# Kernel optimization log

Measured on AMD Instinct MI355X. Metric: run time of the kernel, lower is better.

The kernel has to match this reference:

```python
import jax, jax.numpy as jnp
import numpy as np
import math

DIM = 384
HEADS = 6
HEAD_DIM = DIM // HEADS
MLP_HIDDEN = int(DIM * 2.0)


def layer_norm(x, g, b, eps=1e-5):
    mu = jnp.mean(x, axis=-1, keepdims=True)
    var = jnp.mean((x - mu) ** 2, axis=-1, keepdims=True)
    return (x - mu) * jax.lax.rsqrt(var + eps) * g + b


def setup_inputs() -> dict:
    key = jax.random.key(0)
    ks = jax.random.split(key, 12)
    B, N = 4, 2048
    s = 0.02
    return {
        "x": jax.random.normal(ks[0], (B, N, DIM), dtype=jnp.float32),
        "pos": jax.random.normal(ks[1], (B, N, 3), dtype=jnp.float32),
        "qkv_w": jax.random.normal(ks[2], (DIM, 3 * DIM), dtype=jnp.float32) * s,
        "qkv_b": jnp.zeros((3 * DIM,), jnp.float32),
        "proj_w": jax.random.normal(ks[3], (DIM, DIM), dtype=jnp.float32) * s,
        "proj_b": jnp.zeros((DIM,), jnp.float32),
        "mlp_w1": jax.random.normal(ks[4], (DIM, MLP_HIDDEN), dtype=jnp.float32) * s,
        "mlp_b1": jnp.zeros((MLP_HIDDEN,), jnp.float32),
        "mlp_w2": jax.random.normal(ks[5], (MLP_HIDDEN, DIM), dtype=jnp.float32) * s,
        "mlp_b2": jnp.zeros((DIM,), jnp.float32),
        "ln1_g": jnp.ones((DIM,), jnp.float32),
        "ln1_b": jnp.zeros((DIM,), jnp.float32),
        "ln2_g": jnp.ones((DIM,), jnp.float32),
        "ln2_b": jnp.zeros((DIM,), jnp.float32),
    }


def reference(x, pos, qkv_w, qkv_b, proj_w, proj_b, mlp_w1, mlp_b1,
              mlp_w2, mlp_b2, ln1_g, ln1_b, ln2_g, ln2_b):
    B, N, D = x.shape
    H, Hd = HEADS, HEAD_DIM
    # qkv projection
    qkv = layer_norm(x, ln1_g, ln1_b) @ qkv_w + qkv_b          # [B,N,3D]
    qkv = qkv.reshape(B, N, 3, H, Hd)
    q = jnp.transpose(qkv[:, :, 0], (0, 2, 1, 3))               # [B,H,N,Hd]
    k = jnp.transpose(qkv[:, :, 1], (0, 2, 1, 3))
    v = jnp.transpose(qkv[:, :, 2], (0, 2, 1, 3))
    # pairwise squared-distance bias: exp(-||p_i - p_j||^2)
    rel = pos[:, :, None, :] - pos[:, None, :, :]               # [B,N,N,3]
    dist = jnp.exp(-jnp.sum(rel ** 2, axis=-1))                 # [B,N,N]
    scale = 1.0 / math.sqrt(Hd)
    attn = jnp.einsum('bhqd,bhkd->bhqk', q, k) * scale + dist[:, None, :, :]
    attn = jax.nn.softmax(attn, axis=-1)
    out = jnp.einsum('bhqk,bhkd->bhqd', attn, v)                # [B,H,N,Hd]
    out = jnp.transpose(out, (0, 2, 1, 3)).reshape(B, N, D)
    out = out @ proj_w + proj_b
    x = x + out
    h = layer_norm(x, ln2_g, ln2_b)
    h = jax.nn.gelu(h @ mlp_w1 + mlp_b1, approximate=False) @ mlp_w2 + mlp_b2
    return x + h
```

## Files before the change

kernel.cpp:

```cpp
#include <hip/hip_runtime.h>
#include <hip/hip_bf16.h>
#include <math.h>

#define DIMD 384
#define NHEADS 6
#define HD 64
#define MLPH 768
#define SEQ 2048
#define NBATCH 4
#define NTOK (NBATCH*SEQ)

typedef __hip_bfloat16 bf16;

typedef __attribute__((ext_vector_type(8))) short bf16x8;
typedef __attribute__((ext_vector_type(4))) float f32x4;

#define LOG2E 1.44269504088896340736f

static __device__ inline float fexp2(float x) { return __builtin_amdgcn_exp2f(x); }

static __device__ inline f32x4 mfma16(bf16x8 a, bf16x8 b, f32x4 c) {
    return __builtin_amdgcn_mfma_f32_16x16x32_bf16(a, b, c, 0, 0, 0);
}

static __device__ inline unsigned int cvtpk(float lo, float hi) {
    unsigned int r;
    asm("v_cvt_pk_bf16_f32 %0, %1, %2" : "=v"(r) : "v"(lo), "v"(hi));
    return r;
}
static __device__ inline float bflo(unsigned int u) { return __builtin_bit_cast(float, u << 16); }
static __device__ inline float bfhi(unsigned int u) { return __builtin_bit_cast(float, u & 0xffff0000u); }

static __device__ inline void gld16(const void* g, void* l) {
    __builtin_amdgcn_global_load_lds(
        (const __attribute__((address_space(1))) unsigned int*)g,
        (__attribute__((address_space(3))) unsigned int*)l, 16, 0, 0);
}

__global__ __launch_bounds__(256) void ln_k(const float* __restrict__ x,
                                            const float* __restrict__ gm,
                                            const float* __restrict__ bt,
                                            bf16* __restrict__ out) {
    int row = blockIdx.x * 4 + (threadIdx.x >> 6);
    int l = threadIdx.x & 63;
    const float* xr = x + (size_t)row * DIMD;
    float v[6];
#pragma unroll
    for (int j = 0; j < 6; ++j) v[j] = xr[l + 64 * j];
    float s = 0.f, s2 = 0.f;
#pragma unroll
    for (int j = 0; j < 6; ++j) { s += v[j]; s2 += v[j] * v[j]; }
#pragma unroll
    for (int m = 1; m < 64; m <<= 1) { s += __shfl_xor(s, m); s2 += __shfl_xor(s2, m); }
    float mu = s * (1.f / DIMD);
    float var = s2 * (1.f / DIMD) - mu * mu;
    float rs = rsqrtf(var + 1e-5f);
    bf16* orow = out + (size_t)row * DIMD;
#pragma unroll
    for (int j = 0; j < 6; ++j) {
        int i = l + 64 * j;
        orow[i] = __float2bfloat16((v[j] - mu) * rs * gm[i] + bt[i]);
    }
}

__global__ __launch_bounds__(256) void prep_k(const float* __restrict__ w1,
                                              const float* __restrict__ w2,
                                              const float* __restrict__ w3,
                                              const float* __restrict__ w4,
                                              bf16* __restrict__ o1,
                                              bf16* __restrict__ o2,
                                              bf16* __restrict__ o3,
                                              bf16* __restrict__ o4,
                                              const float* __restrict__ pos,
                                              bf16* __restrict__ DP,
                                              const float* __restrict__ x,
                                              const float* __restrict__ g1,
                                              const float* __restrict__ b1,
                                              bf16* __restrict__ xn) {
    __shared__ float t[32][33];
    int id = blockIdx.x;
    if (id < 1152) {
        const float* W; bf16* O; int K, N;
        if (id < 432)      { W = w1; O = o1; K = 384; N = 1152; }
        else if (id < 576) { W = w2; O = o2; K = 384; N = 384;  id -= 432; }
        else if (id < 864) { W = w3; O = o3; K = 384; N = 768;  id -= 576; }
        else               { W = w4; O = o4; K = 768; N = 384;  id -= 864; }
        int nbx = N >> 5;
        int nb = (id % nbx) * 32, kb = (id / nbx) * 32;
        int tx = threadIdx.x & 31, ty = threadIdx.x >> 5;
#pragma unroll
        for (int i = 0; i < 4; ++i)
            t[ty + 8 * i][tx] = W[(size_t)(kb + ty + 8 * i) * N + nb + tx];
        __syncthreads();
#pragma unroll
        for (int i = 0; i < 4; ++i)
            O[(size_t)(nb + ty + 8 * i) * K + kb + tx] = __float2bfloat16(t[tx][ty + 8 * i]);
    } else if (id < 1664) {
        int blk = id - 1152;
        int w = blk & 3, qt = (blk >> 2) & 31, b = blk >> 7;
        int l = threadIdx.x & 63, tt = threadIdx.x >> 6;
        int lq = l & 15, g = l >> 4;
        int q = qt * 64 + w * 16 + lq;
        const float* pq = pos + ((size_t)b * SEQ + q) * 3;
        float px = pq[0], py = pq[1], pz = pq[2];
        const float* posb = pos + (size_t)b * SEQ * 3;
        char* base = (char*)DP + (size_t)blk * 65536;
        for (int j = 0; j < 8; ++j) {
            int tt8 = tt * 8 + j;
#pragma unroll
            for (int m = 0; m < 2; ++m) {
                int k0 = tt8 * 64 + 32 * m + 4 * g;
                float a[24];
                const float* pk = posb + 3 * k0;
                *(f32x4*)&a[0]  = *(const f32x4*)pk;
                *(f32x4*)&a[4]  = *(const f32x4*)(pk + 4);
                *(f32x4*)&a[8]  = *(const f32x4*)(pk + 8);
                const float* pk2 = posb + 3 * (k0 + 16);
                *(f32x4*)&a[12] = *(const f32x4*)pk2;
                *(f32x4*)&a[16] = *(const f32x4*)(pk2 + 4);
                *(f32x4*)&a[20] = *(const f32x4*)(pk2 + 8);
                float o8[8];
#pragma unroll
                for (int r = 0; r < 8; ++r) {
                    float dx = px - a[3 * r], dy = py - a[3 * r + 1], dz = pz - a[3 * r + 2];
                    o8[r] = fexp2(-LOG2E * (dx * dx + dy * dy + dz * dz)) * LOG2E;
                }
                uint4 o;
                o.x = cvtpk(o8[0], o8[1]); o.y = cvtpk(o8[2], o8[3]);
                o.z = cvtpk(o8[4], o8[5]); o.w = cvtpk(o8[6], o8[7]);
                *(uint4*)(base + ((size_t)tt8 * 2 + m) * 1024 + l * 16) = o;
            }
        }
    } else {
        int row = (id - 1664) * 4 + (threadIdx.x >> 6);
        int l = threadIdx.x & 63;
        const float* xr = x + (size_t)row * DIMD;
        float v[6];
#pragma unroll
        for (int j = 0; j < 6; ++j) v[j] = xr[l + 64 * j];
        float s = 0.f, s2 = 0.f;
#pragma unroll
        for (int j = 0; j < 6; ++j) { s += v[j]; s2 += v[j] * v[j]; }
#pragma unroll
        for (int m = 1; m < 64; m <<= 1) { s += __shfl_xor(s, m); s2 += __shfl_xor(s2, m); }
        float mu = s * (1.f / DIMD);
        float var = s2 * (1.f / DIMD) - mu * mu;
        float rs = rsqrtf(var + 1e-5f);
        bf16* orow = xn + (size_t)row * DIMD;
#pragma unroll
        for (int j = 0; j < 6; ++j) {
            int i = l + 64 * j;
            orow[i] = __float2bfloat16((v[j] - mu) * rs * g1[i] + b1[i]);
        }
    }
}

template <int EPI>
__global__ __launch_bounds__(256) void gemm128_k(const bf16* __restrict__ A,
                                                 const bf16* __restrict__ WT,
                                                 const float* __restrict__ bias,
                                                 bf16* __restrict__ ob0,
                                                 bf16* __restrict__ ob1,
                                                 bf16* __restrict__ ob2,
                                                 int K, int Nw) {
    __shared__ __align__(16) char Als[2][8192];
    __shared__ __align__(16) char Bls[2][8192];
    int tid = threadIdx.x;
    int w = tid >> 6, l = tid & 63;
    int c = l & 15, g = l >> 4;
    int wr = w >> 1, wc = w & 1;
    int m0 = blockIdx.y * 128, n0 = blockIdx.x * 128;
    const char* Ag = (const char*)A + (size_t)m0 * K * 2;
    const char* Bg = (const char*)WT + (size_t)n0 * K * 2;
    int K2 = K * 2;

    f32x4 acc[4][4];
#pragma unroll
    for (int mi = 0; mi < 4; ++mi)
#pragma unroll
        for (int ni = 0; ni < 4; ++ni) acc[mi][ni] = (f32x4){0.f, 0.f, 0.f, 0.f};

    auto stage = [&](int t, int bi) {
#pragma unroll
        for (int p = 0; p < 2; ++p) {
            int chunk = p * 256 + tid;
            int r = chunk >> 2;
            int cc = ((chunk & 3) ^ (r & 3)) << 4;
            gld16(Ag + (size_t)r * K2 + t * 64 + cc, &Als[bi][chunk * 16]);
            gld16(Bg + (size_t)r * K2 + t * 64 + cc, &Bls[bi][chunk * 16]);
        }
    };

    stage(0, 0);
    int kcn = K >> 5;
    for (int t = 0; t < kcn; ++t) {
        int bi = t & 1;
        __syncthreads();
        if (t + 1 < kcn) stage(t + 1, bi ^ 1);
        bf16x8 af[4], bfr[4];
#pragma unroll
        for (int mi = 0; mi < 4; ++mi) {
            int row = wr * 64 + mi * 16 + c;
            __builtin_memcpy(&af[mi], &Als[bi][row * 64 + ((g ^ (row & 3)) << 4)], 16);
        }
#pragma unroll
        for (int ni = 0; ni < 4; ++ni) {
            int row = wc * 64 + ni * 16 + c;
            __builtin_memcpy(&bfr[ni], &Bls[bi][row * 64 + ((g ^ (row & 3)) << 4)], 16);
        }
#pragma unroll
        for (int mi = 0; mi < 4; ++mi)
#pragma unroll
            for (int ni = 0; ni < 4; ++ni)
                acc[mi][ni] = mfma16(af[mi], bfr[ni], acc[mi][ni]);
    }

#pragma unroll
    for (int mi = 0; mi < 4; ++mi) {
#pragma unroll
        for (int ni = 0; ni < 4; ++ni) {
            int ntb = n0 + wc * 64 + ni * 16;
#pragma unroll
            for (int r = 0; r < 4; ++r) {
                int m = m0 + wr * 64 + mi * 16 + 4 * g + r;
                int n = ntb + c;
                float val = acc[mi][ni][r] + bias[n];
                if (EPI == 0) {
                    int which = ntb / DIMD;
                    int rem = ntb - which * DIMD;
                    int h = rem >> 6;
                    int d = (rem & 63) + c;
                    int b = m >> 11, s = m & (SEQ - 1);
                    if (which == 2) {
                        int slot = (s & ~31) + 8 * ((m & 15) >> 2) + 4 * ((m >> 4) & 1) + (m & 3);
                        ob2[(((size_t)b * NHEADS + h) * HD + d) * SEQ + slot] = __float2bfloat16(val);
                    } else {
                        bf16* dp = which == 0 ? ob0 : ob1;
                        dp[(((size_t)b * NHEADS + h) * SEQ + s) * HD + d] = __float2bfloat16(val);
                    }
                } else {
                    float ge = 0.5f * val * (1.0f + erff(val * 0.70710678118654752f));
                    ob0[(size_t)m * Nw + n] = __float2bfloat16(ge);
                }
            }
        }
    }
}

template <int EPI>
__global__ __launch_bounds__(256) void gemm_k(const bf16* __restrict__ A,
                                              const bf16* __restrict__ WT,
                                              const float* __restrict__ bias,
                                              const float* __restrict__ resid,
                                              float* __restrict__ outf,
                                              int K, int Nw) {
    __shared__ __align__(16) char Als[2][8192];
    __shared__ __align__(16) char Bls[2][8192];
    int tid = threadIdx.x;
    int w = tid >> 6, l = tid & 63;
    int c = l & 15, g = l >> 4;
    int m0 = blockIdx.y * 64, n0 = blockIdx.x * 64;
    const char* Ag = (const char*)A + (size_t)m0 * K * 2;
    const char* Bg = (const char*)WT + (size_t)n0 * K * 2;
    int K2 = K * 2;

    f32x4 acc[4];
#pragma unroll
    for (int nt = 0; nt < 4; ++nt) acc[nt] = (f32x4){0.f, 0.f, 0.f, 0.f};

    auto stage = [&](int t, int bi) {
#pragma unroll
        for (int p = 0; p < 2; ++p) {
            int chunk = p * 256 + tid;
            int r = chunk >> 3;
            int cc = ((chunk & 7) ^ (r & 7)) << 4;
            gld16(Ag + (size_t)r * K2 + t * 128 + cc, &Als[bi][chunk * 16]);
            gld16(Bg + (size_t)r * K2 + t * 128 + cc, &Bls[bi][chunk * 16]);
        }
    };

    stage(0, 0);
    int kcn = K >> 6;
    int arow = (16 * w + c) * 128;
    int sw = c & 7;
    for (int t = 0; t < kcn; ++t) {
        int bi = t & 1;
        __syncthreads();
        if (t + 1 < kcn) stage(t + 1, bi ^ 1);
#pragma unroll
        for (int kk = 0; kk < 2; ++kk) {
            int ch = ((kk * 4 + g) ^ sw) << 4;
            bf16x8 af;
            __builtin_memcpy(&af, &Als[bi][arow + ch], 16);
#pragma unroll
            for (int nt = 0; nt < 4; ++nt) {
                bf16x8 bfr;
                __builtin_memcpy(&bfr, &Bls[bi][(nt * 16 + c) * 128 + ch], 16);
                acc[nt] = mfma16(af, bfr, acc[nt]);
            }
        }
    }

#pragma unroll
    for (int nt = 0; nt < 4; ++nt) {
        int ntb = n0 + nt * 16;
#pragma unroll
        for (int r = 0; r < 4; ++r) {
            int m = m0 + 16 * w + 4 * g + r;
            int n = ntb + c;
            float val = acc[nt][r] + bias[n];
            val += resid[(size_t)m * Nw + n];
            outf[(size_t)m * Nw + n] = val;
        }
    }
}

__global__ __launch_bounds__(256) void attn_k(const bf16* __restrict__ q,
                                              const bf16* __restrict__ k,
                                              const bf16* __restrict__ vT,
                                              const bf16* __restrict__ DP,
                                              bf16* __restrict__ out) {
    __shared__ __align__(16) char Kls[3][8192];
    __shared__ __align__(16) char Vls[3][8192];

    int tid = threadIdx.x;
    int w = tid >> 6, l = tid & 63;
    int lq = l & 15, g = l >> 4;
    int qt = blockIdx.x & 31;
    int bh = blockIdx.x >> 5;
    int b = bh / NHEADS, h = bh % NHEADS;
    int qrow = qt * 64 + w * 16 + lq;

    const bf16* qp = q + ((size_t)bh * SEQ + qrow) * HD + 8 * g;
    bf16x8 qf0 = *(const bf16x8*)qp;
    bf16x8 qf1 = *(const bf16x8*)(qp + 32);

    const char* kgb = (const char*)(k + (size_t)bh * SEQ * HD);
    const char* vgb = (const char*)(vT + (size_t)bh * HD * SEQ);
    const char* dpb = (const char*)DP + ((size_t)((b * 32 + qt) * 4 + w)) * 65536 + l * 16;

    const float SC2 = 0.125f * LOG2E;
    f32x4 oacc[4];
#pragma unroll
    for (int dt = 0; dt < 4; ++dt) oacc[dt] = (f32x4){0.f, 0.f, 0.f, 0.f};
    f32x4 osum = (f32x4){0.f, 0.f, 0.f, 0.f};
    bf16x8 ones = {(short)0x3F80, (short)0x3F80, (short)0x3F80, (short)0x3F80,
                   (short)0x3F80, (short)0x3F80, (short)0x3F80, (short)0x3F80};

    auto stage = [&](int t, int bi) {
#pragma unroll
        for (int p = 0; p < 2; ++p) {
            int chunk = p * 256 + tid;
            int r = chunk >> 3, c = chunk & 7;
            int cc = (c ^ (r & 7)) << 4;
            gld16(kgb + (size_t)t * 8192 + r * 128 + cc, &Kls[bi][chunk * 16]);
            gld16(vgb + (size_t)r * 4096 + t * 128 + cc, &Vls[bi][chunk * 16]);
        }
    };

    stage(0, 0);
    uint4 cdp0 = *(const uint4*)(dpb);
    uint4 cdp1 = *(const uint4*)(dpb + 1024);
    stage(1, 1);

    int ib0 = 0, ib1 = 1, ib2 = 2;
    int swq = lq & 7;
    for (int t = 0; t < 32; ++t) {
        asm volatile("s_waitcnt vmcnt(4)" ::: "memory");
        __builtin_amdgcn_sched_barrier(0);
        __builtin_amdgcn_s_barrier();
        __builtin_amdgcn_sched_barrier(0);

        f32x4 st[4];
        __builtin_amdgcn_s_setprio(1);
#pragma unroll
        for (int s = 0; s < 4; ++s) {
            int ro = (16 * s + lq) * 128;
            bf16x8 klo, khi;
            __builtin_memcpy(&klo, &Kls[ib0][ro + ((g ^ swq) << 4)], 16);
            __builtin_memcpy(&khi, &Kls[ib0][ro + (((4 + g) ^ swq) << 4)], 16);
            f32x4 z = (f32x4){0.f, 0.f, 0.f, 0.f};
            st[s] = mfma16(klo, qf0, z);
            st[s] = mfma16(khi, qf1, st[s]);
        }
        __builtin_amdgcn_s_setprio(0);

#pragma unroll
        for (int m = 0; m < 2; ++m) {
            uint4 cd = m == 0 ? cdp0 : cdp1;
            f32x4 s0v = st[2 * m], s1v = st[2 * m + 1];
            float p[8];
            p[0] = fexp2(s0v[0] * SC2 + bflo(cd.x));
            p[1] = fexp2(s0v[1] * SC2 + bfhi(cd.x));
            p[2] = fexp2(s0v[2] * SC2 + bflo(cd.y));
            p[3] = fexp2(s0v[3] * SC2 + bfhi(cd.y));
            p[4] = fexp2(s1v[0] * SC2 + bflo(cd.z));
            p[5] = fexp2(s1v[1] * SC2 + bfhi(cd.z));
            p[6] = fexp2(s1v[2] * SC2 + bflo(cd.w));
            p[7] = fexp2(s1v[3] * SC2 + bfhi(cd.w));

            unsigned int pw[4];
            pw[0] = cvtpk(p[0], p[1]);
            pw[1] = cvtpk(p[2], p[3]);
            pw[2] = cvtpk(p[4], p[5]);
            pw[3] = cvtpk(p[6], p[7]);
            bf16x8 pf;
            __builtin_memcpy(&pf, pw, 16);

            __builtin_amdgcn_s_setprio(1);
            osum = mfma16(ones, pf, osum);
#pragma unroll
            for (int dt = 0; dt < 4; ++dt) {
                int rv = (16 * dt + lq) * 128;
                bf16x8 vf;
                __builtin_memcpy(&vf, &Vls[ib0][rv + (((4 * m + g) ^ swq) << 4)], 16);
                oacc[dt] = mfma16(vf, pf, oacc[dt]);
            }
            __builtin_amdgcn_s_setprio(0);
        }

        __builtin_amdgcn_sched_barrier(0);
        int tn1 = t + 1 < 32 ? t + 1 : 31;
        const char* dpn = dpb + (size_t)tn1 * 2048;
        uint4 ndp0 = *(const uint4*)(dpn);
        uint4 ndp1 = *(const uint4*)(dpn + 1024);
        __builtin_amdgcn_sched_barrier(0);
        int tn2 = t + 2 < 32 ? t + 2 : 31;
        stage(tn2, ib2);
        __builtin_amdgcn_sched_barrier(0);
        cdp0 = ndp0; cdp1 = ndp1;
        int tmp = ib0; ib0 = ib1; ib1 = ib2; ib2 = tmp;
    }

    float inv = 1.f / osum[0];
    bf16* op = out + ((size_t)b * SEQ + qrow) * DIMD + h * HD + 4 * g;
#pragma unroll
    for (int dt = 0; dt < 4; ++dt) {
        unsigned int t2[2];
        t2[0] = cvtpk(oacc[dt][0] * inv, oacc[dt][1] * inv);
        t2[1] = cvtpk(oacc[dt][2] * inv, oacc[dt][3] * inv);
        __builtin_memcpy(op + dt * 16, t2, 8);
    }
}

extern "C" void kernel_launch(void* const* d_in, const int* in_sizes, int n_in,
                              void* d_out, int out_size, void* d_ws, size_t ws_size,
                              hipStream_t stream) {
    const float* x      = (const float*)d_in[0];
    const float* pos    = (const float*)d_in[1];
    const float* qkv_w  = (const float*)d_in[2];
    const float* qkv_b  = (const float*)d_in[3];
    const float* proj_w = (const float*)d_in[4];
    const float* proj_b = (const float*)d_in[5];
    const float* mlp_w1 = (const float*)d_in[6];
    const float* mlp_b1 = (const float*)d_in[7];
    const float* mlp_w2 = (const float*)d_in[8];
    const float* mlp_b2 = (const float*)d_in[9];
    const float* ln1_g  = (const float*)d_in[10];
    const float* ln1_b  = (const float*)d_in[11];
    const float* ln2_g  = (const float*)d_in[12];
    const float* ln2_b  = (const float*)d_in[13];

    char* p = (char*)d_ws;
    size_t off = 0;
    auto alloc = [&](size_t bytes) {
        char* r = p + off;
        off = (off + bytes + 255) & ~(size_t)255;
        return r;
    };
    bf16* WT1 = (bf16*)alloc((size_t)1152 * 384 * 2);
    bf16* WT2 = (bf16*)alloc((size_t)384 * 384 * 2);
    bf16* WT3 = (bf16*)alloc((size_t)384 * 768 * 2);
    bf16* WT4 = (bf16*)alloc((size_t)768 * 384 * 2);
    bf16* xn  = (bf16*)alloc((size_t)NTOK * DIMD * 2);
    bf16* xn2 = (bf16*)alloc((size_t)NTOK * DIMD * 2);
    bf16* qb  = (bf16*)alloc((size_t)NTOK * DIMD * 2);
    bf16* kb  = (bf16*)alloc((size_t)NTOK * DIMD * 2);
    bf16* vTb = (bf16*)alloc((size_t)NTOK * DIMD * 2);
    bf16* ao  = (bf16*)alloc((size_t)NTOK * DIMD * 2);
    float* x1 = (float*)alloc((size_t)NTOK * DIMD * 4);
    bf16* hh  = (bf16*)alloc((size_t)NTOK * MLPH * 2);
    bf16* dtab = (bf16*)alloc((size_t)NBATCH * SEQ * SEQ * 2);
    if (off > ws_size) return;

    prep_k<<<1152 + 512 + 2048, 256, 0, stream>>>(
        qkv_w, proj_w, mlp_w1, mlp_w2, WT1, WT2, WT3, WT4,
        pos, dtab, x, ln1_g, ln1_b, xn);

    gemm128_k<0><<<dim3(1152 / 128, NTOK / 128), 256, 0, stream>>>(
        xn, WT1, qkv_b, qb, kb, vTb, 384, 1152);
    attn_k<<<NBATCH * NHEADS * (SEQ / 64), 256, 0, stream>>>(qb, kb, vTb, dtab, ao);
    gemm_k<1><<<dim3(384 / 64, NTOK / 64), 256, 0, stream>>>(
        ao, WT2, proj_b, x, x1, 384, 384);
    ln_k<<<NTOK / 4, 256, 0, stream>>>(x1, ln2_g, ln2_b, xn2);
    gemm128_k<2><<<dim3(768 / 128, NTOK / 128), 256, 0, stream>>>(
        xn2, WT3, mlp_b1, hh, nullptr, nullptr, 384, 768);
    gemm_k<3><<<dim3(384 / 64, NTOK / 64), 256, 0, stream>>>(
        hh, WT4, mlp_b2, x1, (float*)d_out, 768, 384);
}
```

Baseline: 141.8 us.

## Register-tile two query tiles per wave in attention to reuse K/V LDS fragments

The attention kernel drops from 4 waves per block to 2, and each wave now handles 32 query rows (two 16-row tiles) instead of 16. Each K and V fragment read from LDS now feeds two MFMA streams, which halves LDS read traffic per MFMA. Staging loops and the vmcnt wait count are adjusted for the doubled per-thread copy work, and the unused EPI template parameter is removed from gemm_k. The trade-off is roughly double the accumulator and score registers per wave and half as many resident waves in total, which reduces latency hiding.

```diff
diff --git a/kernel.cpp b/kernel.cpp
--- a/kernel.cpp
+++ b/kernel.cpp
@@ -247,7 +247,6 @@
     }
 }
 
-template <int EPI>
 __global__ __launch_bounds__(256) void gemm_k(const bf16* __restrict__ A,
                                               const bf16* __restrict__ WT,
                                               const float* __restrict__ bias,
@@ -315,7 +314,7 @@
     }
 }
 
-__global__ __launch_bounds__(256) void attn_k(const bf16* __restrict__ q,
+__global__ __launch_bounds__(128) void attn_k(const bf16* __restrict__ q,
                                               const bf16* __restrict__ k,
                                               const bf16* __restrict__ vT,
                                               const bf16* __restrict__ DP,
@@ -329,49 +328,66 @@
     int qt = blockIdx.x & 31;
     int bh = blockIdx.x >> 5;
     int b = bh / NHEADS, h = bh % NHEADS;
-    int qrow = qt * 64 + w * 16 + lq;
-
-    const bf16* qp = q + ((size_t)bh * SEQ + qrow) * HD + 8 * g;
-    bf16x8 qf0 = *(const bf16x8*)qp;
-    bf16x8 qf1 = *(const bf16x8*)(qp + 32);
+    int qrowA = qt * 64 + w * 32 + lq;
+    int qrowB = qrowA + 16;
+
+    const bf16* qpA = q + ((size_t)bh * SEQ + qrowA) * HD + 8 * g;
+    bf16x8 qa0 = *(const bf16x8*)qpA;
+    bf16x8 qa1 = *(const bf16x8*)(qpA + 32);
+    const bf16* qpB = q + ((size_t)bh * SEQ + qrowB) * HD + 8 * g;
+    bf16x8 qb0 = *(const bf16x8*)qpB;
+    bf16x8 qb1 = *(const bf16x8*)(qpB + 32);
 
     const char* kgb = (const char*)(k + (size_t)bh * SEQ * HD);
     const char* vgb = (const char*)(vT + (size_t)bh * HD * SEQ);
-    const char* dpb = (const char*)DP + ((size_t)((b * 32 + qt) * 4 + w)) * 65536 + l * 16;
+    const char* dpA = (const char*)DP + ((size_t)((b * 32 + qt) * 4 + 2 * w)) * 65536 + l * 16;
+    const char* dpB = dpA + 65536;
 
     const float SC2 = 0.125f * LOG2E;
-    f32x4 oacc[4];
-#pragma unroll
-    for (int dt = 0; dt < 4; ++dt) oacc[dt] = (f32x4){0.f, 0.f, 0.f, 0.f};
-    f32x4 osum = (f32x4){0.f, 0.f, 0.f, 0.f};
+    f32x4 oaccA[4], oaccB[4];
+#pragma unroll
+    for (int dt = 0; dt < 4; ++dt) {
+        oaccA[dt] = (f32x4){0.f, 0.f, 0.f, 0.f};
+        oaccB[dt] = (f32x4){0.f, 0.f, 0.f, 0.f};
+    }
+    f32x4 osumA = (f32x4){0.f, 0.f, 0.f, 0.f};
+    f32x4 osumB = osumA;
     bf16x8 ones = {(short)0x3F80, (short)0x3F80, (short)0x3F80, (short)0x3F80,
                    (short)0x3F80, (short)0x3F80, (short)0x3F80, (short)0x3F80};
 
     auto stage = [&](int t, int bi) {
 #pragma unroll
-        for (int p = 0; p < 2; ++p) {
-            int chunk = p * 256 + tid;
+        for (int p = 0; p < 4; ++p) {
+            int chunk = p * 128 + tid;
             int r = chunk >> 3, c = chunk & 7;
             int cc = (c ^ (r & 7)) << 4;
             gld16(kgb + (size_t)t * 8192 + r * 128 + cc, &Kls[bi][chunk * 16]);
+        }
+#pragma unroll
+        for (int p = 0; p < 4; ++p) {
+            int chunk = p * 128 + tid;
+            int r = chunk >> 3, c = chunk & 7;
+            int cc = (c ^ (r & 7)) << 4;
             gld16(vgb + (size_t)r * 4096 + t * 128 + cc, &Vls[bi][chunk * 16]);
         }
     };
 
     stage(0, 0);
-    uint4 cdp0 = *(const uint4*)(dpb);
-    uint4 cdp1 = *(const uint4*)(dpb + 1024);
+    uint4 cdA0 = *(const uint4*)(dpA);
+    uint4 cdA1 = *(const uint4*)(dpA + 1024);
+    uint4 cdB0 = *(const uint4*)(dpB);
+    uint4 cdB1 = *(const uint4*)(dpB + 1024);
     stage(1, 1);
 
     int ib0 = 0, ib1 = 1, ib2 = 2;
     int swq = lq & 7;
     for (int t = 0; t < 32; ++t) {
-        asm volatile("s_waitcnt vmcnt(4)" ::: "memory");
+        asm volatile("s_waitcnt vmcnt(8)" ::: "memory");
         __builtin_amdgcn_sched_barrier(0);
         __builtin_amdgcn_s_barrier();
         __builtin_amdgcn_sched_barrier(0);
 
-        f32x4 st[4];
+        f32x4 stA[4], stB[4];
         __builtin_amdgcn_s_setprio(1);
 #pragma unroll
         for (int s = 0; s < 4; ++s) {
@@ -380,66 +396,89 @@
             __builtin_memcpy(&klo, &Kls[ib0][ro + ((g ^ swq) << 4)], 16);
             __builtin_memcpy(&khi, &Kls[ib0][ro + (((4 + g) ^ swq) << 4)], 16);
             f32x4 z = (f32x4){0.f, 0.f, 0.f, 0.f};
-            st[s] = mfma16(klo, qf0, z);
-            st[s] = mfma16(khi, qf1, st[s]);
+            stA[s] = mfma16(klo, qa0, z);
+            stA[s] = mfma16(khi, qa1, stA[s]);
+            stB[s] = mfma16(klo, qb0, z);
+            stB[s] = mfma16(khi, qb1, stB[s]);
         }
         __builtin_amdgcn_s_setprio(0);
 
 #pragma unroll
         for (int m = 0; m < 2; ++m) {
-            uint4 cd = m == 0 ? cdp0 : cdp1;
-            f32x4 s0v = st[2 * m], s1v = st[2 * m + 1];
-            float p[8];
-            p[0] = fexp2(s0v[0] * SC2 + bflo(cd.x));
-            p[1] = fexp2(s0v[1] * SC2 + bfhi(cd.x));
-            p[2] = fexp2(s0v[2] * SC2 + bflo(cd.y));
-            p[3] = fexp2(s0v[3] * SC2 + bfhi(cd.y));
-            p[4] = fexp2(s1v[0] * SC2 + bflo(cd.z));
-            p[5] = fexp2(s1v[1] * SC2 + bfhi(cd.z));
-            p[6] = fexp2(s1v[2] * SC2 + bflo(cd.w));
-            p[7] = fexp2(s1v[3] * SC2 + bfhi(cd.w));
-
-            unsigned int pw[4];
-            pw[0] = cvtpk(p[0], p[1]);
-            pw[1] = cvtpk(p[2], p[3]);
-            pw[2] = cvtpk(p[4], p[5]);
-            pw[3] = cvtpk(p[6], p[7]);
-            bf16x8 pf;
-            __builtin_memcpy(&pf, pw, 16);
+            uint4 cdA = m == 0 ? cdA0 : cdA1;
+            uint4 cdB = m == 0 ? cdB0 : cdB1;
+            f32x4 sA0 = stA[2 * m], sA1 = stA[2 * m + 1];
+            f32x4 sB0 = stB[2 * m], sB1 = stB[2 * m + 1];
+            float pA[8], pB[8];
+            pA[0] = fexp2(sA0[0] * SC2 + bflo(cdA.x));
+            pA[1] = fexp2(sA0[1] * SC2 + bfhi(cdA.x));
+            pA[2] = fexp2(sA0[2] * SC2 + bflo(cdA.y));
+            pA[3] = fexp2(sA0[3] * SC2 + bfhi(cdA.y));
+            pA[4] = fexp2(sA1[0] * SC2 + bflo(cdA.z));
+            pA[5] = fexp2(sA1[1] * SC2 + bfhi(cdA.z));
+            pA[6] = fexp2(sA1[2] * SC2 + bflo(cdA.w));
+            pA[7] = fexp2(sA1[3] * SC2 + bfhi(cdA.w));
+            pB[0] = fexp2(sB0[0] * SC2 + bflo(cdB.x));
+            pB[1] = fexp2(sB0[1] * SC2 + bfhi(cdB.x));
+            pB[2] = fexp2(sB0[2] * SC2 + bflo(cdB.y));
+            pB[3] = fexp2(sB0[3] * SC2 + bfhi(cdB.y));
+            pB[4] = fexp2(sB1[0] * SC2 + bflo(cdB.z));
+            pB[5] = fexp2(sB1[1] * SC2 + bfhi(cdB.z));
+            pB[6] = fexp2(sB1[2] * SC2 + bflo(cdB.w));
+            pB[7] = fexp2(sB1[3] * SC2 + bfhi(cdB.w));
+
+            unsigned int pwA[4], pwB[4];
+            pwA[0] = cvtpk(pA[0], pA[1]); pwA[1] = cvtpk(pA[2], pA[3]);
+            pwA[2] = cvtpk(pA[4], pA[5]); pwA[3] = cvtpk(pA[6], pA[7]);
+            pwB[0] = cvtpk(pB[0], pB[1]); pwB[1] = cvtpk(pB[2], pB[3]);
+            pwB[2] = cvtpk(pB[4], pB[5]); pwB[3] = cvtpk(pB[6], pB[7]);
+            bf16x8 pfA, pfB;
+            __builtin_memcpy(&pfA, pwA, 16);
+            __builtin_memcpy(&pfB, pwB, 16);
 
             __builtin_amdgcn_s_setprio(1);
-            osum = mfma16(ones, pf, osum);
+            osumA = mfma16(ones, pfA, osumA);
+            osumB = mfma16(ones, pfB, osumB);
 #pragma unroll
             for (int dt = 0; dt < 4; ++dt) {
                 int rv = (16 * dt + lq) * 128;
                 bf16x8 vf;
                 __builtin_memcpy(&vf, &Vls[ib0][rv + (((4 * m + g) ^ swq) << 4)], 16);
-                oacc[dt] = mfma16(vf, pf, oacc[dt]);
+                oaccA[dt] = mfma16(vf, pfA, oaccA[dt]);
+                oaccB[dt] = mfma16(vf, pfB, oaccB[dt]);
             }
             __builtin_amdgcn_s_setprio(0);
         }
 
         __builtin_amdgcn_sched_barrier(0);
         int tn1 = t + 1 < 32 ? t + 1 : 31;
-        const char* dpn = dpb + (size_t)tn1 * 2048;
-        uint4 ndp0 = *(const uint4*)(dpn);
-        uint4 ndp1 = *(const uint4*)(dpn + 1024);
+        const char* dA = dpA + (size_t)tn1 * 2048;
+        const char* dB = dpB + (size_t)tn1 * 2048;
+        uint4 nA0 = *(const uint4*)(dA);
+        uint4 nA1 = *(const uint4*)(dA + 1024);
+        uint4 nB0 = *(const uint4*)(dB);
+        uint4 nB1 = *(const uint4*)(dB + 1024);
         __builtin_amdgcn_sched_barrier(0);
         int tn2 = t + 2 < 32 ? t + 2 : 31;
         stage(tn2, ib2);
         __builtin_amdgcn_sched_barrier(0);
-        cdp0 = ndp0; cdp1 = ndp1;
+        cdA0 = nA0; cdA1 = nA1; cdB0 = nB0; cdB1 = nB1;
         int tmp = ib0; ib0 = ib1; ib1 = ib2; ib2 = tmp;
     }
 
-    float inv = 1.f / osum[0];
-    bf16* op = out + ((size_t)b * SEQ + qrow) * DIMD + h * HD + 4 * g;
+    float invA = 1.f / osumA[0];
+    float invB = 1.f / osumB[0];
+    bf16* opA = out + ((size_t)b * SEQ + qrowA) * DIMD + h * HD + 4 * g;
+    bf16* opB = out + ((size_t)b * SEQ + qrowB) * DIMD + h * HD + 4 * g;
 #pragma unroll
     for (int dt = 0; dt < 4; ++dt) {
         unsigned int t2[2];
-        t2[0] = cvtpk(oacc[dt][0] * inv, oacc[dt][1] * inv);
-        t2[1] = cvtpk(oacc[dt][2] * inv, oacc[dt][3] * inv);
-        __builtin_memcpy(op + dt * 16, t2, 8);
+        t2[0] = cvtpk(oaccA[dt][0] * invA, oaccA[dt][1] * invA);
+        t2[1] = cvtpk(oaccA[dt][2] * invA, oaccA[dt][3] * invA);
+        __builtin_memcpy(opA + dt * 16, t2, 8);
+        t2[0] = cvtpk(oaccB[dt][0] * invB, oaccB[dt][1] * invB);
+        t2[1] = cvtpk(oaccB[dt][2] * invB, oaccB[dt][3] * invB);
+        __builtin_memcpy(opB + dt * 16, t2, 8);
     }
 }
 
@@ -489,12 +528,12 @@
 
     gemm128_k<0><<<dim3(1152 / 128, NTOK / 128), 256, 0, stream>>>(
         xn, WT1, qkv_b, qb, kb, vTb, 384, 1152);
-    attn_k<<<NBATCH * NHEADS * (SEQ / 64), 256, 0, stream>>>(qb, kb, vTb, dtab, ao);
-    gemm_k<1><<<dim3(384 / 64, NTOK / 64), 256, 0, stream>>>(
+    attn_k<<<NBATCH * NHEADS * (SEQ / 64), 128, 0, stream>>>(qb, kb, vTb, dtab, ao);
+    gemm_k<<<dim3(384 / 64, NTOK / 64), 256, 0, stream>>>(
         ao, WT2, proj_b, x, x1, 384, 384);
     ln_k<<<NTOK / 4, 256, 0, stream>>>(x1, ln2_g, ln2_b, xn2);
     gemm128_k<2><<<dim3(768 / 128, NTOK / 128), 256, 0, stream>>>(
         xn2, WT3, mlp_b1, hh, nullptr, nullptr, 384, 768);
-    gemm_k<3><<<dim3(384 / 64, NTOK / 64), 256, 0, stream>>>(
+    gemm_k<<<dim3(384 / 64, NTOK / 64), 256, 0, stream>>>(
         hh, WT4, mlp_b2, x1, (float*)d_out, 768, 384);
 }
```

New measurement: 150.7 us. 6.3% more time.
